# Performance work log

Hardware: AMD Instinct MI355X
Metric: run time of the kernel (lower is better)

## Reference

```python
import jax, jax.numpy as jnp
import numpy as np

B, T, D, H = 32, 2048, 256, 256  # batch, length, input_size, hidden_size


def _lstm_layer(x, W_ih, W_hh, b, reverse):
    """Single-direction LSTM over time. x: [B,T,Din]; W_ih: [4H,Din]; W_hh: [4H,H]; b: [4H].
    Gate order: i, f, g, o (PyTorch convention). Returns hidden states [B,T,H]."""
    # Precompute input contribution for all timesteps in one big GEMM.
    xg = jnp.einsum('btd,gd->btg', x, W_ih) + b  # [B,T,4H]
    Hh = W_hh.shape[1]
    Bb = x.shape[0]

    def step(carry, xg_t):
        h, c = carry
        g = xg_t + h @ W_hh.T  # [B,4H]
        i, f, gc, o = jnp.split(g, 4, axis=-1)
        c = jax.nn.sigmoid(f) * c + jax.nn.sigmoid(i) * jnp.tanh(gc)
        h = jax.nn.sigmoid(o) * jnp.tanh(c)
        return (h, c), h

    init = (jnp.zeros((Bb, Hh), x.dtype), jnp.zeros((Bb, Hh), x.dtype))
    _, hs = jax.lax.scan(step, init, jnp.swapaxes(xg, 0, 1), reverse=reverse)  # [T,B,H]
    return jnp.swapaxes(hs, 0, 1)  # [B,T,H]


def setup_inputs() -> dict:
    key = jax.random.key(0)
    ks = jax.random.split(key, 13)
    s = 0.05
    G = 4 * H
    inp = {
        'x': jax.random.normal(ks[0], (B, T, D), dtype=jnp.float32),
        # layer 0 (input size D), forward and reverse directions
        'W_ih_f0': jax.random.normal(ks[1], (G, D), dtype=jnp.float32) * s,
        'W_hh_f0': jax.random.normal(ks[2], (G, H), dtype=jnp.float32) * s,
        'b_f0': jnp.zeros((G,), dtype=jnp.float32),
        'W_ih_r0': jax.random.normal(ks[3], (G, D), dtype=jnp.float32) * s,
        'W_hh_r0': jax.random.normal(ks[4], (G, H), dtype=jnp.float32) * s,
        'b_r0': jnp.zeros((G,), dtype=jnp.float32),
        # layer 1 (input size 2H because bidirectional)
        'W_ih_f1': jax.random.normal(ks[5], (G, 2 * H), dtype=jnp.float32) * s,
        'W_hh_f1': jax.random.normal(ks[6], (G, H), dtype=jnp.float32) * s,
        'b_f1': jnp.zeros((G,), dtype=jnp.float32),
        'W_ih_r1': jax.random.normal(ks[7], (G, 2 * H), dtype=jnp.float32) * s,
        'W_hh_r1': jax.random.normal(ks[8], (G, H), dtype=jnp.float32) * s,
        'b_r1': jnp.zeros((G,), dtype=jnp.float32),
    }
    return inp


def reference(x, W_ih_f0, W_hh_f0, b_f0, W_ih_r0, W_hh_r0, b_r0,
              W_ih_f1, W_hh_f1, b_f1, W_ih_r1, W_hh_r1, b_r1):
    # Layer 0: bidirectional over raw input
    h0 = jnp.concatenate([
        _lstm_layer(x, W_ih_f0, W_hh_f0, b_f0, reverse=False),
        _lstm_layer(x, W_ih_r0, W_hh_r0, b_r0, reverse=True),
    ], axis=-1)  # [B,T,2H]
    # Layer 1: bidirectional over concatenated hidden states
    h1 = jnp.concatenate([
        _lstm_layer(h0, W_ih_f1, W_hh_f1, b_f1, reverse=False),
        _lstm_layer(h0, W_ih_r1, W_hh_r1, b_r1, reverse=True),
    ], axis=-1)  # [B,T,2H]
    return h1
```

## Files before the change

kernel.cpp:

```cpp
#include <hip/hip_runtime.h>
#include <stdint.h>


#define Bn 32
#define Tn 2048
#define Hn 256

typedef short short8 __attribute__((ext_vector_type(8)));
typedef float f32x4 __attribute__((ext_vector_type(4)));

__device__ inline unsigned short f2b(float f) {
  union { float f; unsigned u; } v; v.f = f;
  unsigned r = v.u + 0x7fffu + ((v.u >> 16) & 1u);
  return (unsigned short)(r >> 16);
}
__device__ inline float b2f(unsigned short b) {
  union { unsigned u; float f; } v; v.u = ((unsigned)b) << 16;
  return v.f;
}
__device__ inline float sigx(float x) {
  return __builtin_amdgcn_rcpf(1.f + __expf(-x));
}
__device__ inline float tanhx(float x) {
  return 2.f * __builtin_amdgcn_rcpf(1.f + __expf(-2.f * x)) - 1.f;
}

template <int K, bool AF32>
__global__ __launch_bounds__(256, 2) void xg_gemm(
    const void* __restrict__ Ain,
    const float* __restrict__ Wf, const float* __restrict__ bf_,
    const float* __restrict__ Wr, const float* __restrict__ br_,
    unsigned short* __restrict__ xg) {
  constexpr int KI = K / 32;
  const int bid = blockIdx.x;
  const int scan = bid & 1;
  const int sgrp = (bid >> 1) & 7;
  const int mchunk = bid >> 4;
  const int wave = threadIdx.x >> 6;
  const int lane = threadIdx.x & 63;
  const int l15 = lane & 15, quad = lane >> 4;
  const int stripe = sgrp * 4 + wave;
  const int gi0 = stripe * 32;

  const float* W = scan ? Wr : Wf;
  const float* bias = scan ? br_ : bf_;

  short8 bfr[KI][2];
  float bias2[2];
#pragma unroll
  for (int sub = 0; sub < 2; ++sub) {
    const int gi = gi0 + sub * 16 + l15;
    bias2[sub] = bias[gi];
#pragma unroll
    for (int ki = 0; ki < KI; ++ki) {
      const float* src = W + (size_t)gi * K + ki * 32 + quad * 8;
      short8 v;
#pragma unroll
      for (int j = 0; j < 8; ++j) v[j] = (short)f2b(src[j]);
      bfr[ki][sub] = v;
    }
  }

  const size_t scan_off = (size_t)scan << 26;
#pragma unroll 1
  for (int mt0 = 0; mt0 < 16; ++mt0) {
    const int mt = mchunk * 16 + mt0;
    const size_t row = (size_t)mt * 16 + l15;
    f32x4 acc[2];
#pragma unroll
    for (int sub = 0; sub < 2; ++sub) {
      f32x4 bi = {bias2[sub], bias2[sub], bias2[sub], bias2[sub]};
      acc[sub] = bi;
    }
#pragma unroll
    for (int ki = 0; ki < KI; ++ki) {
      short8 af;
      if constexpr (AF32) {
        const float* ap = (const float*)Ain + row * K + ki * 32 + quad * 8;
        f32x4 a0 = *(const f32x4*)ap;
        f32x4 a1 = *(const f32x4*)(ap + 4);
#pragma unroll
        for (int j = 0; j < 4; ++j) { af[j] = (short)f2b(a0[j]); af[4 + j] = (short)f2b(a1[j]); }
      } else {
        const unsigned short* ap = (const unsigned short*)Ain + row * K + ki * 32 + quad * 8;
        af = *(const short8*)ap;
      }
#pragma unroll
      for (int sub = 0; sub < 2; ++sub)
        acc[sub] = __builtin_amdgcn_mfma_f32_16x16x32_bf16(af, bfr[ki][sub], acc[sub], 0, 0, 0);
    }
#pragma unroll
    for (int sub = 0; sub < 2; ++sub) {
      const int gi = gi0 + sub * 16 + l15;
#pragma unroll
      for (int r = 0; r < 4; ++r) {
        const int orow = mt * 16 + quad * 4 + r;
        const int m = orow >> 11, t = orow & 2047;
        xg[scan_off + ((size_t)t * Bn + m) * 1024 + gi] = f2b(acc[sub][r]);
      }
    }
  }
}

template <bool LAYER1>
__global__ __launch_bounds__(256, 1) void lstm_scan(
    const unsigned short* __restrict__ xg,
    const float* __restrict__ Whh_f, const float* __restrict__ Whh_r,
    unsigned short* __restrict__ hbuf,
    int* __restrict__ flags,
    unsigned short* __restrict__ h0out,
    float* __restrict__ dout) {
  const int bid = blockIdx.x;
  const int scan = bid & 1;
  const int wg = bid >> 1;
  const int wave = threadIdx.x >> 6;
  const int lane = threadIdx.x & 63;
  const int slot = wg * 4 + wave;
  const int cg = slot >> 1, mh = slot & 1;
  const int l15 = lane & 15, quad = lane >> 4;
  const int U = cg * 16 + l15;
  const int mrow = mh * 16 + l15;

  const float* Whh = scan ? Whh_r : Whh_f;

  short8 bfh[8][4];
#pragma unroll
  for (int ki = 0; ki < 8; ++ki) {
#pragma unroll
    for (int g = 0; g < 4; ++g) {
      const float* src = Whh + (size_t)(g * Hn + U) * Hn + ki * 32 + quad * 8;
      short8 v;
#pragma unroll
      for (int j = 0; j < 8; ++j) v[j] = (short)f2b(src[j]);
      bfh[ki][g] = v;
    }
  }

  unsigned short* myhb = hbuf + scan * (2 * Bn * Hn);
  int* myflags = flags + scan * 32;
  const size_t scan_off = (size_t)scan << 26;

  float c_st[4] = {0.f, 0.f, 0.f, 0.f};

  for (int s = 0; s < Tn; ++s) {
    const int t = scan ? (Tn - 1 - s) : s;

    const unsigned short* xgp = xg + scan_off + (size_t)t * (Bn * 1024);
    f32x4 acc[4];
#pragma unroll
    for (int g = 0; g < 4; ++g) {
#pragma unroll
      for (int r = 0; r < 4; ++r) {
        const int m = mh * 16 + quad * 4 + r;
        acc[g][r] = b2f(xgp[m * 1024 + g * Hn + U]);
      }
    }

    if (s > 0) {
      for (;;) {
        int v = (lane < 32)
                  ? __hip_atomic_load(&myflags[lane], __ATOMIC_RELAXED, __HIP_MEMORY_SCOPE_AGENT)
                  : s;
        if (__all(v >= s)) break;
        __builtin_amdgcn_s_sleep(1);
      }
      const unsigned long long* hq = (const unsigned long long*)myhb;
      const int pbase = ((s - 1) & 1) * 2048 + mrow * 64;
#pragma unroll
      for (int ki = 0; ki < 8; ++ki) {
        const int idx = pbase + ki * 8 + quad * 2;
        unsigned long long q0 = __hip_atomic_load(hq + idx, __ATOMIC_RELAXED, __HIP_MEMORY_SCOPE_AGENT);
        unsigned long long q1 = __hip_atomic_load(hq + idx + 1, __ATOMIC_RELAXED, __HIP_MEMORY_SCOPE_AGENT);
        union { unsigned long long q[2]; short8 s8; } u;
        u.q[0] = q0; u.q[1] = q1;
#pragma unroll
        for (int g = 0; g < 4; ++g)
          acc[g] = __builtin_amdgcn_mfma_f32_16x16x32_bf16(u.s8, bfh[ki][g], acc[g], 0, 0, 0);
      }
    }

    unsigned int* hw32 = (unsigned int*)(myhb + (s & 1) * (Bn * Hn));
#pragma unroll
    for (int r = 0; r < 4; ++r) {
      const int m = mh * 16 + quad * 4 + r;
      float ig = sigx(acc[0][r]), fg = sigx(acc[1][r]);
      float gg = tanhx(acc[2][r]), og = sigx(acc[3][r]);
      float cv = fg * c_st[r] + ig * gg;
      c_st[r] = cv;
      float hv = og * tanhx(cv);
      unsigned short hb16 = f2b(hv);
      int pk = __shfl_xor((int)hb16, 1);
      if (!(lane & 1)) {
        unsigned int pv = (unsigned)hb16 | ((unsigned)pk << 16);
        __hip_atomic_store(hw32 + m * 128 + (U >> 1), pv, __ATOMIC_RELAXED, __HIP_MEMORY_SCOPE_AGENT);
      }
      if constexpr (!LAYER1) {
        h0out[((size_t)m * Tn + t) * 512 + scan * Hn + U] = hb16;
      } else {
        dout[((size_t)m * Tn + t) * 512 + scan * Hn + U] = hv;
      }
    }

    asm volatile("s_waitcnt vmcnt(0)" ::: "memory");
    if (lane == 0)
      __hip_atomic_store(&myflags[slot], s + 1, __ATOMIC_RELAXED, __HIP_MEMORY_SCOPE_AGENT);
  }
}

extern "C" void kernel_launch(void* const* d_in, const int* in_sizes, int n_in,
                              void* d_out, int out_size, void* d_ws, size_t ws_size,
                              hipStream_t stream) {
  (void)in_sizes; (void)n_in; (void)out_size; (void)ws_size;
  const float* x      = (const float*)d_in[0];
  const float* Wih_f0 = (const float*)d_in[1];
  const float* Whh_f0 = (const float*)d_in[2];
  const float* b_f0   = (const float*)d_in[3];
  const float* Wih_r0 = (const float*)d_in[4];
  const float* Whh_r0 = (const float*)d_in[5];
  const float* b_r0   = (const float*)d_in[6];
  const float* Wih_f1 = (const float*)d_in[7];
  const float* Whh_f1 = (const float*)d_in[8];
  const float* b_f1   = (const float*)d_in[9];
  const float* Wih_r1 = (const float*)d_in[10];
  const float* Whh_r1 = (const float*)d_in[11];
  const float* b_r1   = (const float*)d_in[12];

  char* ws = (char*)d_ws;
  unsigned short* xgbuf = (unsigned short*)ws;
  size_t off = (size_t)2 * Tn * Bn * 1024 * sizeof(unsigned short);
  unsigned short* h0out = (unsigned short*)(ws + off);
  off += (size_t)Bn * Tn * 512 * sizeof(unsigned short);
  unsigned short* hbufA = (unsigned short*)(ws + off); off += 2 * 2 * Bn * Hn * 2;
  unsigned short* hbufB = (unsigned short*)(ws + off); off += 2 * 2 * Bn * Hn * 2;
  int* flagsA = (int*)(ws + off);
  int* flagsB = flagsA + 64;

  hipMemsetAsync(flagsA, 0, 512, stream);

  dim3 blk(256);
  xg_gemm<256, true><<<dim3(4096), blk, 0, stream>>>(
      (const void*)x, Wih_f0, b_f0, Wih_r0, b_r0, xgbuf);
  lstm_scan<false><<<dim3(16), blk, 0, stream>>>(
      xgbuf, Whh_f0, Whh_r0, hbufA, flagsA, h0out, (float*)nullptr);
  xg_gemm<512, false><<<dim3(4096), blk, 0, stream>>>(
      (const void*)h0out, Wih_f1, b_f1, Wih_r1, b_r1, xgbuf);
  lstm_scan<true><<<dim3(16), blk, 0, stream>>>(
      xgbuf, Whh_f1, Whh_r1, hbufB, flagsB, (unsigned short*)nullptr, (float*)d_out);
}
```

Measured before the change: 16.54 ms.

## Embed step tags in h exchange words to drop separate flag synchronization

Each packed pair of bf16 hidden values is stored as a 64-bit word with the step counter in the upper half, so readers poll the data itself instead of a flag array. This removes the vmcnt wait and extra flag store/load round trip per timestep in the latency-bound recurrence. The input-gate buffer is relaid out as [t][unit][batch][gate] so each lane fetches its gate pre-activations with two vector loads. It doubles the exchanged bytes and relies on stale tags in uninitialized workspace never matching the current step.

```diff
diff --git a/kernel.cpp b/kernel.cpp
--- a/kernel.cpp
+++ b/kernel.cpp
@@ -92,11 +92,12 @@
 #pragma unroll
     for (int sub = 0; sub < 2; ++sub) {
       const int gi = gi0 + sub * 16 + l15;
+      const int g = gi >> 8, u = gi & 255;
 #pragma unroll
       for (int r = 0; r < 4; ++r) {
         const int orow = mt * 16 + quad * 4 + r;
         const int m = orow >> 11, t = orow & 2047;
-        xg[scan_off + ((size_t)t * Bn + m) * 1024 + gi] = f2b(acc[sub][r]);
+        xg[scan_off + (((size_t)t * 256 + u) * 32 + m) * 4 + g] = f2b(acc[sub][r]);
       }
     }
   }
@@ -106,8 +107,7 @@
 __global__ __launch_bounds__(256, 1) void lstm_scan(
     const unsigned short* __restrict__ xg,
     const float* __restrict__ Whh_f, const float* __restrict__ Whh_r,
-    unsigned short* __restrict__ hbuf,
-    int* __restrict__ flags,
+    unsigned long long* __restrict__ hq,
     unsigned short* __restrict__ h0out,
     float* __restrict__ dout) {
   const int bid = blockIdx.x;
@@ -136,8 +136,7 @@
     }
   }
 
-  unsigned short* myhb = hbuf + scan * (2 * Bn * Hn);
-  int* myflags = flags + scan * 32;
+  unsigned long long* myq = hq + (size_t)scan * 8192;
   const size_t scan_off = (size_t)scan << 26;
 
   float c_st[4] = {0.f, 0.f, 0.f, 0.f};
@@ -145,41 +144,54 @@
   for (int s = 0; s < Tn; ++s) {
     const int t = scan ? (Tn - 1 - s) : s;
 
-    const unsigned short* xgp = xg + scan_off + (size_t)t * (Bn * 1024);
+    const unsigned short* xgp =
+        xg + scan_off + (((size_t)t * 256 + U) * 32 + mh * 16 + quad * 4) * 4;
+    short8 x0 = *(const short8*)xgp;
+    short8 x1 = *(const short8*)(xgp + 8);
+
+    unsigned long long q[8][4];
+    if (s > 0) {
+      const unsigned long long* src =
+          myq + (size_t)((s - 1) & 1) * 4096 + (size_t)mrow * 128;
+      bool ok;
+      do {
+#pragma unroll
+        for (int ki = 0; ki < 8; ++ki)
+#pragma unroll
+          for (int n = 0; n < 4; ++n)
+            q[ki][n] = __hip_atomic_load(src + ki * 16 + quad * 4 + n,
+                                         __ATOMIC_RELAXED, __HIP_MEMORY_SCOPE_AGENT);
+        ok = true;
+#pragma unroll
+        for (int ki = 0; ki < 8; ++ki)
+#pragma unroll
+          for (int n = 0; n < 4; ++n)
+            ok &= ((unsigned)(q[ki][n] >> 32) == (unsigned)s);
+      } while (!__all(ok));
+    }
+
     f32x4 acc[4];
 #pragma unroll
     for (int g = 0; g < 4; ++g) {
-#pragma unroll
-      for (int r = 0; r < 4; ++r) {
-        const int m = mh * 16 + quad * 4 + r;
-        acc[g][r] = b2f(xgp[m * 1024 + g * Hn + U]);
-      }
+      f32x4 a = {b2f((unsigned short)x0[g]), b2f((unsigned short)x0[4 + g]),
+                 b2f((unsigned short)x1[g]), b2f((unsigned short)x1[4 + g])};
+      acc[g] = a;
     }
 
     if (s > 0) {
-      for (;;) {
-        int v = (lane < 32)
-                  ? __hip_atomic_load(&myflags[lane], __ATOMIC_RELAXED, __HIP_MEMORY_SCOPE_AGENT)
-                  : s;
-        if (__all(v >= s)) break;
-        __builtin_amdgcn_s_sleep(1);
-      }
-      const unsigned long long* hq = (const unsigned long long*)myhb;
-      const int pbase = ((s - 1) & 1) * 2048 + mrow * 64;
 #pragma unroll
       for (int ki = 0; ki < 8; ++ki) {
-        const int idx = pbase + ki * 8 + quad * 2;
-        unsigned long long q0 = __hip_atomic_load(hq + idx, __ATOMIC_RELAXED, __HIP_MEMORY_SCOPE_AGENT);
-        unsigned long long q1 = __hip_atomic_load(hq + idx + 1, __ATOMIC_RELAXED, __HIP_MEMORY_SCOPE_AGENT);
-        union { unsigned long long q[2]; short8 s8; } u;
-        u.q[0] = q0; u.q[1] = q1;
+        union { unsigned u[4]; short8 s8; } uu;
+#pragma unroll
+        for (int n = 0; n < 4; ++n) uu.u[n] = (unsigned)q[ki][n];
 #pragma unroll
         for (int g = 0; g < 4; ++g)
-          acc[g] = __builtin_amdgcn_mfma_f32_16x16x32_bf16(u.s8, bfh[ki][g], acc[g], 0, 0, 0);
-      }
-    }
-
-    unsigned int* hw32 = (unsigned int*)(myhb + (s & 1) * (Bn * Hn));
+          acc[g] = __builtin_amdgcn_mfma_f32_16x16x32_bf16(uu.s8, bfh[ki][g], acc[g], 0, 0, 0);
+      }
+    }
+
+    float hvals[4];
+    unsigned long long* dst = myq + (size_t)(s & 1) * 4096;
 #pragma unroll
     for (int r = 0; r < 4; ++r) {
       const int m = mh * 16 + quad * 4 + r;
@@ -188,22 +200,25 @@
       float cv = fg * c_st[r] + ig * gg;
       c_st[r] = cv;
       float hv = og * tanhx(cv);
+      hvals[r] = hv;
       unsigned short hb16 = f2b(hv);
-      int pk = __shfl_xor((int)hb16, 1);
+      unsigned pk = ((unsigned)__shfl_xor((int)hb16, 1)) & 0xffffu;
       if (!(lane & 1)) {
-        unsigned int pv = (unsigned)hb16 | ((unsigned)pk << 16);
-        __hip_atomic_store(hw32 + m * 128 + (U >> 1), pv, __ATOMIC_RELAXED, __HIP_MEMORY_SCOPE_AGENT);
-      }
-      if constexpr (!LAYER1) {
-        h0out[((size_t)m * Tn + t) * 512 + scan * Hn + U] = hb16;
-      } else {
-        dout[((size_t)m * Tn + t) * 512 + scan * Hn + U] = hv;
-      }
-    }
-
-    asm volatile("s_waitcnt vmcnt(0)" ::: "memory");
-    if (lane == 0)
-      __hip_atomic_store(&myflags[slot], s + 1, __ATOMIC_RELAXED, __HIP_MEMORY_SCOPE_AGENT);
+        unsigned pair = (unsigned)hb16 | (pk << 16);
+        unsigned long long v = (((unsigned long long)(unsigned)(s + 1)) << 32) | pair;
+        __hip_atomic_store(dst + m * 128 + (U >> 1), v,
+                           __ATOMIC_RELAXED, __HIP_MEMORY_SCOPE_AGENT);
+      }
+    }
+
+#pragma unroll
+    for (int r = 0; r < 4; ++r) {
+      const int m = mh * 16 + quad * 4 + r;
+      if constexpr (!LAYER1)
+        h0out[((size_t)m * Tn + t) * 512 + scan * Hn + U] = f2b(hvals[r]);
+      else
+        dout[((size_t)m * Tn + t) * 512 + scan * Hn + U] = hvals[r];
+    }
   }
 }
 
@@ -230,20 +245,16 @@
   size_t off = (size_t)2 * Tn * Bn * 1024 * sizeof(unsigned short);
   unsigned short* h0out = (unsigned short*)(ws + off);
   off += (size_t)Bn * Tn * 512 * sizeof(unsigned short);
-  unsigned short* hbufA = (unsigned short*)(ws + off); off += 2 * 2 * Bn * Hn * 2;
-  unsigned short* hbufB = (unsigned short*)(ws + off); off += 2 * 2 * Bn * Hn * 2;
-  int* flagsA = (int*)(ws + off);
-  int* flagsB = flagsA + 64;
-
-  hipMemsetAsync(flagsA, 0, 512, stream);
+  unsigned long long* hqA = (unsigned long long*)(ws + off); off += 2 * 8192 * 8;
+  unsigned long long* hqB = (unsigned long long*)(ws + off); off += 2 * 8192 * 8;
 
   dim3 blk(256);
   xg_gemm<256, true><<<dim3(4096), blk, 0, stream>>>(
       (const void*)x, Wih_f0, b_f0, Wih_r0, b_r0, xgbuf);
   lstm_scan<false><<<dim3(16), blk, 0, stream>>>(
-      xgbuf, Whh_f0, Whh_r0, hbufA, flagsA, h0out, (float*)nullptr);
+      xgbuf, Whh_f0, Whh_r0, hqA, h0out, (float*)nullptr);
   xg_gemm<512, false><<<dim3(4096), blk, 0, stream>>>(
       (const void*)h0out, Wih_f1, b_f1, Wih_r1, b_r1, xgbuf);
   lstm_scan<true><<<dim3(16), blk, 0, stream>>>(
-      xgbuf, Whh_f1, Whh_r1, hbufB, flagsB, (unsigned short*)nullptr, (float*)d_out);
-}
+      xgbuf, Whh_f1, Whh_r1, hqB, (unsigned short*)nullptr, (float*)d_out);
+}
```

Measured after the change: 28.06 ms. 1.7x slower.
